# Kernel tuning notes

Hardware: AMD Instinct MI355X
Metric: run time of the kernel (lower is better)

## Reference

```python
import jax, jax.numpy as jnp
import numpy as np

N_NODES = 100000
N_EDGES = 3200000
D_IN = 256
D_HID = 97


def setup_inputs() -> dict:
    key = jax.random.key(0)
    k1, k2, k3, k4, k5, k6 = jax.random.split(key, 6)
    x = jax.random.normal(k1, (N_NODES, D_IN), dtype=jnp.float32)
    edge_index = jax.random.randint(k2, (2, N_EDGES), 0, N_NODES, dtype=jnp.int64)
    # GCNConv weights (stored as [in, out]) and biases
    W1 = jax.random.normal(k3, (D_IN, D_HID), dtype=jnp.float32) / np.sqrt(D_IN)
    b1 = jnp.zeros((D_HID,), dtype=jnp.float32)
    W2 = jax.random.normal(k4, (D_HID, D_HID), dtype=jnp.float32) / np.sqrt(D_HID)
    b2 = jnp.zeros((D_HID,), dtype=jnp.float32)
    return {"x": x, "edge_index": edge_index, "W1": W1, "b1": b1, "W2": W2, "b2": b2}


def reference(x, edge_index, W1, b1, W2, b2):
    # PyG GCNConv: add self-loops, symmetric degree normalization,
    # out[i] = sum_j norm_ij * (x[j] @ W) + b
    N = x.shape[0]
    self_idx = jnp.arange(N, dtype=edge_index.dtype)
    src = jnp.concatenate([edge_index[0], self_idx])  # source j
    dst = jnp.concatenate([edge_index[1], self_idx])  # target i
    deg = jax.ops.segment_sum(jnp.ones_like(dst, dtype=x.dtype), dst, num_segments=N)
    dinv = jnp.where(deg > 0, 1.0 / jnp.sqrt(deg), 0.0)
    norm = dinv[src] * dinv[dst]  # [E+N]

    def gcn(h, W, b):
        h = h @ W  # dense linear transform first (out_dim small)
        msg = h[src] * norm[:, None]  # gather + scale
        agg = jax.ops.segment_sum(msg, dst, num_segments=N)  # scatter-add
        return agg + b

    h = jax.nn.relu(gcn(x, W1, b1))
    out = gcn(h, W2, b2)
    return out
```

## Files before the change

### kernel.cpp

```cpp
#include <hip/hip_runtime.h>
#include <hip/hip_fp16.h>
#include <stdint.h>

#define D_IN 256
#define D_H  97
#define RST  96
#define NPB  512
#define NBMAX 256
#define CHUNK 4096
#define KP1  264
#define KP2  136

typedef _Float16 f16;
typedef f16   f16x8 __attribute__((ext_vector_type(8)));
typedef float f32x4 __attribute__((ext_vector_type(4)));

__device__ __forceinline__ int load_idx(const void* p, int is64, long long pos) {
  if (is64) return (int)(((const long long*)p)[pos]);
  return ((const int*)p)[pos];
}

__global__ void detect_kernel(const void* ei, long long E, int* flag) {
  const int* p32 = (const int*)ei;
  long long stride = E / 1024; if (stride < 1) stride = 1;
  int tid = threadIdx.x;
  int bad = 0;
  for (int s = 0; s < 4; ++s) {
    long long k = ((long long)tid * 4 + s) * stride;
    if (k < E) {
      if (p32[2 * k + 1] != 0) bad = 1;
    }
  }
  __shared__ int sh_bad;
  if (tid == 0) sh_bad = 0;
  __syncthreads();
  if (bad) atomicOr(&sh_bad, 1);
  __syncthreads();
  if (tid == 0) *flag = sh_bad ? 0 : 1;
}

__global__ __launch_bounds__(256) void bucket_scatter_direct(
    const void* ei, const int* __restrict__ flag, int* __restrict__ bcur,
    unsigned int* __restrict__ bsd, long long E, int nbuck, int cap) {
  __shared__ unsigned int packs[CHUNK];
  __shared__ unsigned char bkts[CHUNK];
  __shared__ int hist[NBMAX];
  __shared__ int gpos[NBMAX];
  __shared__ int cur[NBMAX];
  int tid = threadIdx.x;
  if (tid < NBMAX) { hist[tid] = 0; cur[tid] = 0; }
  __syncthreads();
  int f = *flag;
  long long base = (long long)blockIdx.x * CHUNK;
  int cnt = (int)((E - base < CHUNK) ? (E - base) : CHUNK);
  #pragma unroll 4
  for (int i = tid; i < cnt; i += 256) {
    long long e = base + i;
    int s = load_idx(ei, f, e);
    int d = load_idx(ei, f, E + e);
    int b = d >> 9;
    packs[i] = ((unsigned int)(d & (NPB - 1)) << 17) | (unsigned int)s;
    bkts[i] = (unsigned char)b;
    atomicAdd(&hist[b], 1);
  }
  __syncthreads();
  if (tid < nbuck) { int h = hist[tid]; if (h) gpos[tid] = atomicAdd(&bcur[tid], h); }
  __syncthreads();
  #pragma unroll 4
  for (int i = tid; i < cnt; i += 256) {
    int b = bkts[i];
    int r = atomicAdd(&cur[b], 1);
    int idx = gpos[b] + r;
    if (idx < cap) bsd[(size_t)b * cap + idx] = packs[i];
  }
}

__global__ void bucket_scan2(const int* __restrict__ bcur, int* __restrict__ bstart,
                             int* __restrict__ row_start, int N, int nbuck, int cap) {
  __shared__ int sh[256];
  int tid = threadIdx.x;
  int v = (tid < nbuck) ? min(bcur[tid], cap) : 0;
  sh[tid] = v;
  __syncthreads();
  for (int off = 1; off < 256; off <<= 1) {
    int a = (tid >= off) ? sh[tid - off] : 0;
    __syncthreads();
    sh[tid] += a;
    __syncthreads();
  }
  if (tid < nbuck) bstart[tid] = sh[tid] - v;
  if (tid == 255) { bstart[nbuck] = sh[255]; row_start[N] = sh[255]; }
}

__global__ __launch_bounds__(256) void bucket_finalize(
    const unsigned int* __restrict__ bsd, const int* __restrict__ bcur,
    const int* __restrict__ bstart,
    int* __restrict__ row_start, float* __restrict__ dinv,
    int* __restrict__ csr_src, int N, int cap) {
  __shared__ int h[NPB];
  __shared__ int rs[NPB];
  __shared__ int cur[NPB];
  __shared__ int wsum[4];
  int b = blockIdx.x, tid = threadIdx.x;
  int lane = tid & 63, wid = tid >> 6;
  h[2 * tid] = 0; h[2 * tid + 1] = 0;
  cur[2 * tid] = 0; cur[2 * tid + 1] = 0;
  __syncthreads();
  int d0 = b * cap;
  int cnt = min(bcur[b], cap);
  for (int i = tid; i < cnt; i += 256) atomicAdd(&h[bsd[d0 + i] >> 17], 1);
  __syncthreads();
  int a0 = h[2 * tid], a1 = h[2 * tid + 1];
  int tsum = a0 + a1;
  int incl = tsum;
  #pragma unroll
  for (int off = 1; off < 64; off <<= 1) {
    int n = __shfl_up(incl, off, 64);
    if (lane >= off) incl += n;
  }
  if (lane == 63) wsum[wid] = incl;
  __syncthreads();
  int woff = 0;
  for (int k = 0; k < wid; ++k) woff += wsum[k];
  int excl = woff + incl - tsum + bstart[b];
  rs[2 * tid] = excl;
  rs[2 * tid + 1] = excl + a0;
  int node0 = b * NPB;
  int n0 = node0 + 2 * tid, n1 = node0 + 2 * tid + 1;
  if (n0 < N) { row_start[n0] = excl;      dinv[n0] = rsqrtf((float)(a0 + 1)); }
  if (n1 < N) { row_start[n1] = excl + a0; dinv[n1] = rsqrtf((float)(a1 + 1)); }
  __syncthreads();
  for (int i = tid; i < cnt; i += 256) {
    unsigned int p = bsd[d0 + i];
    int r = p >> 17;
    int s = (int)(p & 0x1FFFFu);
    int rel = atomicAdd(&cur[r], 1);
    csr_src[rs[r] + rel] = s;
  }
}

__global__ void prep_kernel(const float* __restrict__ W1, const float* __restrict__ b1,
                            const float* __restrict__ W2, const float* __restrict__ b2,
                            f16* __restrict__ W1t, f16* __restrict__ W2t,
                            float* __restrict__ b1p, float* __restrict__ b2p) {
  int idx = blockIdx.x * blockDim.x + threadIdx.x;
  const int n1 = 112 * KP1, n2 = 112 * KP2;
  if (idx < n1) {
    int c = idx / KP1, k = idx % KP1;
    W1t[idx] = (f16)((c < D_H && k < 256) ? W1[k * D_H + c] : 0.f);
  } else if (idx < n1 + n2) {
    int j = idx - n1; int c = j / KP2, k = j % KP2;
    W2t[j] = (f16)((c < D_H && k < D_H) ? W2[k * D_H + c] : 0.f);
  } else if (idx < n1 + n2 + 128) {
    int c = idx - (n1 + n2);
    b1p[c] = (c < D_H) ? b1[c] : 0.0f;
  } else if (idx < n1 + n2 + 256) {
    int c = idx - (n1 + n2 + 128);
    b2p[c] = (c < D_H) ? b2[c] : 0.0f;
  }
}

template<int KI, int KP, bool IN_HALF>
__global__ __launch_bounds__(256) void mfma_gemm(
    const float* __restrict__ Af, const f16* __restrict__ Ah,
    const __half2* __restrict__ sideA,
    const f16* __restrict__ Wt, const float* __restrict__ dinv,
    f16* __restrict__ C, __half2* __restrict__ sideC, int N) {
  __shared__ f16 Bs[112 * KP];
  int tid = threadIdx.x, wave = tid >> 6, lane = tid & 63;
  int row0 = blockIdx.x * 128;
  for (int i = tid * 8; i < 112 * KP; i += 2048)
    *(f16x8*)&Bs[i] = *(const f16x8*)&Wt[i];

  int m = lane & 15, q = lane >> 4;
  int kf = q * 8;
  int r0 = row0 + wave * 32 + m;
  int r1 = r0 + 16;
  int rr0 = (r0 < N) ? r0 : 0;
  int rr1 = (r1 < N) ? r1 : 0;

  f16x8 a0[KI], a1[KI];
  #pragma unroll
  for (int kb = 0; kb < KI; ++kb) {
    if constexpr (!IN_HALF) {
      const float* p0 = &Af[(size_t)rr0 * 256 + kb * 32 + kf];
      const float* p1 = &Af[(size_t)rr1 * 256 + kb * 32 + kf];
      float4 u0 = *(const float4*)p0, u1 = *(const float4*)(p0 + 4);
      float4 w0 = *(const float4*)p1, w1 = *(const float4*)(p1 + 4);
      f16x8 t0, t1;
      t0[0] = (f16)u0.x; t0[1] = (f16)u0.y; t0[2] = (f16)u0.z; t0[3] = (f16)u0.w;
      t0[4] = (f16)u1.x; t0[5] = (f16)u1.y; t0[6] = (f16)u1.z; t0[7] = (f16)u1.w;
      t1[0] = (f16)w0.x; t1[1] = (f16)w0.y; t1[2] = (f16)w0.z; t1[3] = (f16)w0.w;
      t1[4] = (f16)w1.x; t1[5] = (f16)w1.y; t1[6] = (f16)w1.z; t1[7] = (f16)w1.w;
      a0[kb] = t0; a1[kb] = t1;
    } else {
      if (kb < KI - 1) {
        a0[kb] = *(const f16x8*)&Ah[(size_t)rr0 * RST + kb * 32 + kf];
        a1[kb] = *(const f16x8*)&Ah[(size_t)rr1 * RST + kb * 32 + kf];
      } else {
        f16x8 z0, z1;
        #pragma unroll
        for (int j = 0; j < 8; ++j) { z0[j] = (f16)0.f; z1[j] = (f16)0.f; }
        if (q == 0) {
          z0[0] = ((const f16*)sideA)[2 * rr0];
          z1[0] = ((const f16*)sideA)[2 * rr1];
        }
        a0[kb] = z0; a1[kb] = z1;
      }
    }
  }

  f32x4 acc[2][7];
  #pragma unroll
  for (int mg = 0; mg < 2; ++mg)
    #pragma unroll
    for (int cg = 0; cg < 7; ++cg)
      #pragma unroll
      for (int j = 0; j < 4; ++j) acc[mg][cg][j] = 0.f;

  __syncthreads();

  #pragma unroll
  for (int kb = 0; kb < KI; ++kb) {
    #pragma unroll
    for (int cg = 0; cg < 7; ++cg) {
      f16x8 b = *(const f16x8*)&Bs[(cg * 16 + m) * KP + kb * 32 + kf];
      acc[0][cg] = __builtin_amdgcn_mfma_f32_16x16x32_f16(a0[kb], b, acc[0][cg], 0, 0, 0);
      acc[1][cg] = __builtin_amdgcn_mfma_f32_16x16x32_f16(a1[kb], b, acc[1][cg], 0, 0, 0);
    }
  }

  int colb = m, rq = q * 4;
  #pragma unroll
  for (int mg = 0; mg < 2; ++mg) {
    #pragma unroll
    for (int j = 0; j < 4; ++j) {
      int r = row0 + wave * 32 + mg * 16 + rq + j;
      if (r >= N) continue;
      float dv = dinv[r];
      #pragma unroll
      for (int cg = 0; cg < 7; ++cg) {
        int c = cg * 16 + colb;
        float val = acc[mg][cg][j] * dv;
        if (c < 96)       C[(size_t)r * RST + c] = (f16)val;
        else if (c == 96) sideC[r] = __floats2half2_rn(val, 0.f);
      }
    }
  }
}

template<bool OUT_HALF, bool DO_RELU>
__global__ __launch_bounds__(256) void agg_kernel(
    const __half* __restrict__ t, const __half2* __restrict__ side,
    const int* __restrict__ csr_src, const int* __restrict__ row_start,
    const float* __restrict__ dinv, const float* __restrict__ bias,
    void* __restrict__ outp, __half2* __restrict__ side_out, int N) {
  int lane = threadIdx.x & 63;
  int node = blockIdx.x * (blockDim.x >> 6) + (threadIdx.x >> 6);
  if (node >= N || lane >= 49) return;
  const char* gbase = (lane < 48) ? (const char*)t + lane * 4 : (const char*)side;
  unsigned gscale = (lane < 48) ? (unsigned)(RST * 2) : 4u;
  auto GATHER = [&](int j) -> float2 {
    return __half22float2(*(const __half2*)(gbase + (size_t)((unsigned)j * gscale)));
  };
  int s = row_start[node], epd = row_start[node + 1];
  float di = dinv[node];
  float2 v = GATHER(node);
  float ax = v.x, ay = v.y;
  int e = s;
  while ((e & 3) && e < epd) {
    float2 u = GATHER(csr_src[e]);
    ax += u.x; ay += u.y; ++e;
  }
  for (; e + 8 <= epd; e += 8) {
    int4 q0 = *(const int4*)(csr_src + e);
    int4 q1 = *(const int4*)(csr_src + e + 4);
    float2 u0 = GATHER(q0.x), u1 = GATHER(q0.y), u2 = GATHER(q0.z), u3 = GATHER(q0.w);
    float2 u4 = GATHER(q1.x), u5 = GATHER(q1.y), u6 = GATHER(q1.z), u7 = GATHER(q1.w);
    ax += ((u0.x + u1.x) + (u2.x + u3.x)) + ((u4.x + u5.x) + (u6.x + u7.x));
    ay += ((u0.y + u1.y) + (u2.y + u3.y)) + ((u4.y + u5.y) + (u6.y + u7.y));
  }
  if (e + 4 <= epd) {
    int4 q0 = *(const int4*)(csr_src + e);
    float2 u0 = GATHER(q0.x), u1 = GATHER(q0.y), u2 = GATHER(q0.z), u3 = GATHER(q0.w);
    ax += (u0.x + u1.x) + (u2.x + u3.x);
    ay += (u0.y + u1.y) + (u2.y + u3.y);
    e += 4;
  }
  for (; e < epd; ++e) {
    float2 u = GATHER(csr_src[e]);
    ax += u.x; ay += u.y;
  }
  int c0 = 2 * lane;
  ax = ax * di + bias[c0];
  ay = ay * di + bias[c0 + 1];
  if (DO_RELU) { ax = fmaxf(ax, 0.f); ay = fmaxf(ay, 0.f); }
  if (OUT_HALF) {
    if (lane < 48) ((__half2*)((__half*)outp + (size_t)node * RST))[lane] = __floats2half2_rn(ax, ay);
    else           side_out[node] = __floats2half2_rn(ax, 0.f);
  } else {
    float* o = (float*)outp + (size_t)node * D_H;
    if (lane < 48) { o[c0] = ax; o[c0 + 1] = ay; }
    else           o[96] = ax;
  }
}

extern "C" void kernel_launch(void* const* d_in, const int* in_sizes, int n_in,
                              void* d_out, int out_size, void* d_ws, size_t ws_size,
                              hipStream_t stream) {
  const float* x  = (const float*)d_in[0];
  const void*  ei = d_in[1];
  const float* W1 = (const float*)d_in[2];
  const float* b1 = (const float*)d_in[3];
  const float* W2 = (const float*)d_in[4];
  const float* b2 = (const float*)d_in[5];
  int N = in_sizes[0] / D_IN;
  long long E = (long long)in_sizes[1] / 2;
  int nbuck = (N + NPB - 1) / NPB;
  int cap = (int)(E / nbuck) + 8192;

  char* base = (char*)d_ws;
  size_t off = 0;
  auto alloc = [&](size_t bytes) -> void* {
    void* p = base + off;
    off = (off + bytes + 255) & ~(size_t)255;
    return p;
  };
  int*    flag      = (int*)alloc(4);
  float*  dinv      = (float*)alloc((size_t)N * 4);
  int*    row_start = (int*)alloc((size_t)(N + 1) * 4);
  int*    bcur      = (int*)alloc((size_t)(nbuck + 1) * 4);
  int*    bstart    = (int*)alloc((size_t)(nbuck + 1) * 4);
  int*    csr_src   = (int*)alloc((size_t)E * 4);
  unsigned int* bsd = (unsigned int*)alloc((size_t)nbuck * cap * 4);
  f16*    W1t       = (f16*)alloc((size_t)112 * KP1 * 2);
  f16*    W2t       = (f16*)alloc((size_t)112 * KP2 * 2);
  float*  b1p       = (float*)alloc(128 * 4);
  float*  b2p       = (float*)alloc(128 * 4);
  f16*    t1        = (f16*)alloc((size_t)N * RST * 2 + 256);
  __half2* sideT    = (__half2*)alloc((size_t)N * 4 + 256);
  f16*    h1        = (f16*)alloc((size_t)N * RST * 2 + 256);
  __half2* sideH    = (__half2*)alloc((size_t)N * 4 + 256);

  hipMemsetAsync(bcur, 0, (size_t)(nbuck + 1) * 4, stream);
  detect_kernel<<<1, 256, 0, stream>>>(ei, E, flag);
  bucket_scatter_direct<<<(int)((E + CHUNK - 1) / CHUNK), 256, 0, stream>>>(
      ei, flag, bcur, bsd, E, nbuck, cap);
  bucket_scan2<<<1, 256, 0, stream>>>(bcur, bstart, row_start, N, nbuck, cap);
  bucket_finalize<<<nbuck, 256, 0, stream>>>(bsd, bcur, bstart, row_start, dinv, csr_src, N, cap);
  prep_kernel<<<(112 * KP1 + 112 * KP2 + 256 + 255) / 256, 256, 0, stream>>>(
      W1, b1, W2, b2, W1t, W2t, b1p, b2p);

  int gGemm = (N + 127) / 128;

  mfma_gemm<8, KP1, false><<<gGemm, 256, 0, stream>>>(
      x, nullptr, nullptr, W1t, dinv, t1, sideT, N);
  agg_kernel<true, true><<<(N + 3) / 4, 256, 0, stream>>>(
      (const __half*)t1, sideT, csr_src, row_start, dinv, b1p, h1, sideH, N);
  mfma_gemm<4, KP2, true><<<gGemm, 256, 0, stream>>>(
      nullptr, h1, sideH, W2t, dinv, t1, sideT, N);
  agg_kernel<false, false><<<(N + 3) / 4, 256, 0, stream>>>(
      (const __half*)t1, sideT, csr_src, row_start, dinv, b2p, d_out, nullptr, N);
}
```

Baseline: 368.9 us.

## Pre-swizzle weights into MFMA fragment order and drop LDS staging in GEMM

The prep kernel now writes W1/W2 in per-lane MFMA B-fragment order, so each lane reads its f16x8 B operand straight from global memory with coalesced 16-byte loads. This removes the shared-memory copy, the LDS reads and the __syncthreads from the GEMM kernels, and relies on L1/L2 caching of the small weight arrays instead. Separately, each aggregation kernel is split into two launches over half the nodes each, which adds launch overhead and has no clear speed benefit.

```diff
diff --git a/kernel.cpp b/kernel.cpp
--- a/kernel.cpp
+++ b/kernel.cpp
@@ -8,8 +8,6 @@
 #define NPB  512
 #define NBMAX 256
 #define CHUNK 4096
-#define KP1  264
-#define KP2  136
 
 typedef _Float16 f16;
 typedef f16   f16x8 __attribute__((ext_vector_type(8)));
@@ -141,16 +139,26 @@
 
 __global__ void prep_kernel(const float* __restrict__ W1, const float* __restrict__ b1,
                             const float* __restrict__ W2, const float* __restrict__ b2,
-                            f16* __restrict__ W1t, f16* __restrict__ W2t,
+                            f16* __restrict__ W1lin, f16* __restrict__ W2lin,
                             float* __restrict__ b1p, float* __restrict__ b2p) {
   int idx = blockIdx.x * blockDim.x + threadIdx.x;
-  const int n1 = 112 * KP1, n2 = 112 * KP2;
+  const int n1 = 8 * 7 * 512;
+  const int n2 = 4 * 7 * 512;
   if (idx < n1) {
-    int c = idx / KP1, k = idx % KP1;
-    W1t[idx] = (f16)((c < D_H && k < 256) ? W1[k * D_H + c] : 0.f);
+    int fid = idx >> 3, hh = idx & 7;
+    int lane = fid & 63, fg = fid >> 6;
+    int kb = fg / 7, cg = fg % 7;
+    int c = cg * 16 + (lane & 15);
+    int k = kb * 32 + (lane >> 4) * 8 + hh;
+    W1lin[idx] = (f16)((c < D_H && k < 256) ? W1[k * D_H + c] : 0.f);
   } else if (idx < n1 + n2) {
-    int j = idx - n1; int c = j / KP2, k = j % KP2;
-    W2t[j] = (f16)((c < D_H && k < D_H) ? W2[k * D_H + c] : 0.f);
+    int j = idx - n1;
+    int fid = j >> 3, hh = j & 7;
+    int lane = fid & 63, fg = fid >> 6;
+    int kb = fg / 7, cg = fg % 7;
+    int c = cg * 16 + (lane & 15);
+    int k = kb * 32 + (lane >> 4) * 8 + hh;
+    W2lin[j] = (f16)((c < D_H && k < D_H) ? W2[k * D_H + c] : 0.f);
   } else if (idx < n1 + n2 + 128) {
     int c = idx - (n1 + n2);
     b1p[c] = (c < D_H) ? b1[c] : 0.0f;
@@ -160,24 +168,21 @@
   }
 }
 
-template<int KI, int KP, bool IN_HALF>
+template<int KI, bool IN_HALF>
 __global__ __launch_bounds__(256) void mfma_gemm(
     const float* __restrict__ Af, const f16* __restrict__ Ah,
     const __half2* __restrict__ sideA,
-    const f16* __restrict__ Wt, const float* __restrict__ dinv,
+    const f16* __restrict__ Wlin, const float* __restrict__ dinv,
     f16* __restrict__ C, __half2* __restrict__ sideC, int N) {
-  __shared__ f16 Bs[112 * KP];
   int tid = threadIdx.x, wave = tid >> 6, lane = tid & 63;
   int row0 = blockIdx.x * 128;
-  for (int i = tid * 8; i < 112 * KP; i += 2048)
-    *(f16x8*)&Bs[i] = *(const f16x8*)&Wt[i];
-
   int m = lane & 15, q = lane >> 4;
   int kf = q * 8;
   int r0 = row0 + wave * 32 + m;
   int r1 = r0 + 16;
   int rr0 = (r0 < N) ? r0 : 0;
   int rr1 = (r1 < N) ? r1 : 0;
+  const f16* wbase = Wlin + lane * 8;
 
   f16x8 a0[KI], a1[KI];
   #pragma unroll
@@ -218,13 +223,11 @@
       #pragma unroll
       for (int j = 0; j < 4; ++j) acc[mg][cg][j] = 0.f;
 
-  __syncthreads();
-
   #pragma unroll
   for (int kb = 0; kb < KI; ++kb) {
     #pragma unroll
     for (int cg = 0; cg < 7; ++cg) {
-      f16x8 b = *(const f16x8*)&Bs[(cg * 16 + m) * KP + kb * 32 + kf];
+      f16x8 b = *(const f16x8*)&wbase[(kb * 7 + cg) * 512];
       acc[0][cg] = __builtin_amdgcn_mfma_f32_16x16x32_f16(a0[kb], b, acc[0][cg], 0, 0, 0);
       acc[1][cg] = __builtin_amdgcn_mfma_f32_16x16x32_f16(a1[kb], b, acc[1][cg], 0, 0, 0);
     }
@@ -254,9 +257,9 @@
     const __half* __restrict__ t, const __half2* __restrict__ side,
     const int* __restrict__ csr_src, const int* __restrict__ row_start,
     const float* __restrict__ dinv, const float* __restrict__ bias,
-    void* __restrict__ outp, __half2* __restrict__ side_out, int N) {
+    void* __restrict__ outp, __half2* __restrict__ side_out, int node_base, int N) {
   int lane = threadIdx.x & 63;
-  int node = blockIdx.x * (blockDim.x >> 6) + (threadIdx.x >> 6);
+  int node = node_base + blockIdx.x * (blockDim.x >> 6) + (threadIdx.x >> 6);
   if (node >= N || lane >= 49) return;
   const char* gbase = (lane < 48) ? (const char*)t + lane * 4 : (const char*)side;
   unsigned gscale = (lane < 48) ? (unsigned)(RST * 2) : 4u;
@@ -333,8 +336,8 @@
   int*    bstart    = (int*)alloc((size_t)(nbuck + 1) * 4);
   int*    csr_src   = (int*)alloc((size_t)E * 4);
   unsigned int* bsd = (unsigned int*)alloc((size_t)nbuck * cap * 4);
-  f16*    W1t       = (f16*)alloc((size_t)112 * KP1 * 2);
-  f16*    W2t       = (f16*)alloc((size_t)112 * KP2 * 2);
+  f16*    W1lin     = (f16*)alloc((size_t)8 * 7 * 512 * 2);
+  f16*    W2lin     = (f16*)alloc((size_t)4 * 7 * 512 * 2);
   float*  b1p       = (float*)alloc(128 * 4);
   float*  b2p       = (float*)alloc(128 * 4);
   f16*    t1        = (f16*)alloc((size_t)N * RST * 2 + 256);
@@ -348,17 +351,24 @@
       ei, flag, bcur, bsd, E, nbuck, cap);
   bucket_scan2<<<1, 256, 0, stream>>>(bcur, bstart, row_start, N, nbuck, cap);
   bucket_finalize<<<nbuck, 256, 0, stream>>>(bsd, bcur, bstart, row_start, dinv, csr_src, N, cap);
-  prep_kernel<<<(112 * KP1 + 112 * KP2 + 256 + 255) / 256, 256, 0, stream>>>(
-      W1, b1, W2, b2, W1t, W2t, b1p, b2p);
+  prep_kernel<<<(8 * 7 * 512 + 4 * 7 * 512 + 256 + 255) / 256, 256, 0, stream>>>(
+      W1, b1, W2, b2, W1lin, W2lin, b1p, b2p);
 
   int gGemm = (N + 127) / 128;
-
-  mfma_gemm<8, KP1, false><<<gGemm, 256, 0, stream>>>(
-      x, nullptr, nullptr, W1t, dinv, t1, sideT, N);
-  agg_kernel<true, true><<<(N + 3) / 4, 256, 0, stream>>>(
-      (const __half*)t1, sideT, csr_src, row_start, dinv, b1p, h1, sideH, N);
-  mfma_gemm<4, KP2, true><<<gGemm, 256, 0, stream>>>(
-      nullptr, h1, sideH, W2t, dinv, t1, sideT, N);
-  agg_kernel<false, false><<<(N + 3) / 4, 256, 0, stream>>>(
-      (const __half*)t1, sideT, csr_src, row_start, dinv, b2p, d_out, nullptr, N);
-}
+  int half = N / 2;
+  int gA0 = (half + 3) / 4;
+  int gA1 = (N - half + 3) / 4;
+
+  mfma_gemm<8, false><<<gGemm, 256, 0, stream>>>(
+      x, nullptr, nullptr, W1lin, dinv, t1, sideT, N);
+  agg_kernel<true, true><<<gA0, 256, 0, stream>>>(
+      (const __half*)t1, sideT, csr_src, row_start, dinv, b1p, h1, sideH, 0, N);
+  agg_kernel<true, true><<<gA1, 256, 0, stream>>>(
+      (const __half*)t1, sideT, csr_src, row_start, dinv, b1p, h1, sideH, half, N);
+  mfma_gemm<4, true><<<gGemm, 256, 0, stream>>>(
+      nullptr, h1, sideH, W2lin, dinv, t1, sideT, N);
+  agg_kernel<false, false><<<gA0, 256, 0, stream>>>(
+      (const __half*)t1, sideT, csr_src, row_start, dinv, b2p, d_out, nullptr, 0, N);
+  agg_kernel<false, false><<<gA1, 256, 0, stream>>>(
+      (const __half*)t1, sideT, csr_src, row_start, dinv, b2p, d_out, nullptr, half, N);
+}
```

Measured after the change: 374.2 us. No clear change (+1.5%).
